# Kernel optimization log

Measured on AMD Instinct MI355X. Metric: run time of the kernel, lower is better.

Reference implementation:

```python
import jax, jax.numpy as jnp
import numpy as np

N_NODES = 30522
HID = 768
N_EDGES = 488352
B, S = 4, 512
L = 12  # transformer_layers
C = 100  # num classes in pos-neg codebook graph


def setup_inputs() -> dict:
    key = jax.random.key(0)
    ks = jax.random.split(key, 20)
    inp = {}
    inp["word_embs"] = jax.random.normal(ks[0], (N_NODES, HID), dtype=jnp.float32)
    inp["input_ids"] = jax.random.randint(ks[1], (B, S), 0, N_NODES + 1)  # N_NODES = padding row
    inp["class_ids"] = jax.random.randint(ks[2], (B, S), 0, C + 1)
    inp["mask"] = jax.random.randint(ks[3], (B, S, 1), 0, 2).astype(bool)
    inp["co_edge_index"] = jax.random.randint(ks[4], (2, N_EDGES), 0, N_NODES)
    inp["co_edge_weight"] = jax.random.uniform(ks[5], (N_EDGES,), dtype=jnp.float32)
    inp["re_edge_index"] = jax.random.randint(ks[6], (2, N_EDGES), 0, N_NODES)
    inp["re_edge_weight"] = jax.random.uniform(ks[7], (N_EDGES,), dtype=jnp.float32)
    pn_graph = jax.random.uniform(ks[8], (C + 1, N_NODES), dtype=jnp.float32) * 0.01
    inp["pn_graph"] = pn_graph.at[-1].set(0.0)  # padding row of zeros
    sc = 0.02
    inp["co_W"] = jax.random.normal(ks[9], (3, HID, HID), dtype=jnp.float32) * sc
    inp["co_b"] = jnp.zeros((3, HID), jnp.float32)
    inp["re_W"] = jax.random.normal(ks[10], (3, HID, HID), dtype=jnp.float32) * sc
    inp["re_b"] = jnp.zeros((3, HID), jnp.float32)
    inp["pn_W"] = jax.random.normal(ks[11], (HID, HID), dtype=jnp.float32) * sc  # [out,in] 1x1 conv
    inp["pn_b"] = jnp.zeros((HID,), jnp.float32)
    # zero_convs are zero-initialized in the original; use small random so math is non-trivial
    inp["zero_w"] = jax.random.normal(ks[12], (L, HID, HID), dtype=jnp.float32) * sc
    inp["zero_b"] = jnp.zeros((L, HID), jnp.float32)
    inp["zero_w_pos"] = jax.random.normal(ks[13], (L, HID, HID), dtype=jnp.float32) * sc
    inp["zero_b_pos"] = jnp.zeros((L, HID), jnp.float32)
    return inp


def _gcn_layer(x, src, dst, ew, W, b, n):
    # PyG GCNConv: add self-loops (weight 1), symmetric normalization
    deg = jax.ops.segment_sum(ew, dst, num_segments=n) + 1.0
    dinv = jnp.where(deg > 0, jax.lax.rsqrt(deg), 0.0)
    norm = dinv[src] * ew * dinv[dst]  # [E]
    h = x @ W  # [n, H]
    agg = jax.ops.segment_sum(norm[:, None] * h[src], dst, num_segments=n)
    agg = agg + h * (dinv * dinv)[:, None]  # self-loop contribution
    return agg + b


def _gcn_stack(x, edge_index, ew, Ws, bs, ids):
    src, dst = edge_index[0], edge_index[1]
    n = x.shape[0]
    h = x
    acc = None
    for i in range(3):
        h = jax.nn.relu(_gcn_layer(h, src, dst, ew, Ws[i], bs[i], n))
        pad = jnp.concatenate([h, jnp.zeros((1, h.shape[-1]), h.dtype)], axis=0)
        g = pad[ids]  # [B, S, H] gather with padding row
        acc = g if acc is None else acc + g
    return acc / 3.0


def _zero_conv_layers(tok, w, b):
    # 1x1 conv over hidden channels for each of L layers: [B,S,H] x [L,O,H] -> [L,B,S,O]
    return jnp.einsum("bsh,loh->lbso", tok, w) + b[:, None, None, :]


def reference(word_embs, input_ids, class_ids, mask,
              co_edge_index, co_edge_weight, re_edge_index, re_edge_weight,
              pn_graph, co_W, co_b, re_W, re_b, pn_W, pn_b,
              zero_w, zero_b, zero_w_pos, zero_b_pos):
    Bq, Sq = input_ids.shape
    H = word_embs.shape[-1]
    Lq = zero_w.shape[0]
    inv_mask = (~mask).astype(word_embs.dtype)  # [B,S,1]
    zero_pad = jnp.zeros((Lq, Bq, 1, H), word_embs.dtype)

    co = _gcn_stack(word_embs, co_edge_index, co_edge_weight, co_W, co_b, input_ids)  # [B,S,H]
    re = _gcn_stack(word_embs, re_edge_index, re_edge_weight, re_W, re_b, input_ids)

    # NOTE: original uses self.zero_convs (not a separate set) for BOTH co and re
    co_l = _zero_conv_layers(co, zero_w, zero_b) * inv_mask[None]
    re_l = _zero_conv_layers(re, zero_w, zero_b) * inv_mask[None]
    co_l = jnp.concatenate([zero_pad, co_l], axis=2)  # [L,B,S+1,H]
    re_l = jnp.concatenate([zero_pad, re_l], axis=2)

    # PosNegCodebook: 1x1 conv on codebook, then dense-graph matmul, gathered by class
    cb = word_embs @ pn_W.T + pn_b  # [N, H]
    pn = (pn_graph @ cb)[class_ids]  # [B,S,H] (same math as graph[class_ids] @ cb)
    pn_l = _zero_conv_layers(pn, zero_w_pos, zero_b_pos)
    pn_l = jnp.concatenate([zero_pad, pn_l], axis=2)

    return (co_l, re_l, pn_l)
```

## Files before the change

kernel.cpp:

```cpp
#include <hip/hip_runtime.h>
#include <stdint.h>

typedef unsigned int u32;
typedef unsigned short u16;
typedef __attribute__((ext_vector_type(8))) short short8;
typedef __attribute__((ext_vector_type(4))) float f32x4;

#define N_NODESC 30522
#define HIDC 768
#define NEC 488352
#define TOKM 2048
#define LLAY 12
#define NCLS 101
#define M_PAD 30720
#define ZNC (LLAY*HIDC)
#define OUT_SET (LLAY*4*513*HIDC)
#define PN_KCHUNK 512
#define NBLK 120
#define NN1 (N_NODESC+1)
#define G4_LDS 65536
#define G8_LDS 131072

__device__ __forceinline__ float bl(u32 u){ return __uint_as_float(u<<16); }
__device__ __forceinline__ float bh(u32 u){ return __uint_as_float(u & 0xffff0000u); }
__device__ __forceinline__ u32 f2b1(float f){ u32 x=__float_as_uint(f); return (x + 0x7fffu + ((x>>16)&1u))>>16; }
__device__ __forceinline__ u32 pack2(float a, float b){ return f2b1(a) | (f2b1(b)<<16); }

__device__ __forceinline__ void mfma16(f32x4& d, short8 a, short8 b){
  asm volatile("v_mfma_f32_16x16x32_bf16 %0, %1, %2, %0" : "+v"(d) : "v"(a), "v"(b));
}
__device__ __forceinline__ void async16(const void* g, void* l){
  __builtin_amdgcn_global_load_lds((const __attribute__((address_space(1))) u32*)g,
                                   (__attribute__((address_space(3))) u32*)l, 16, 0, 0);
}

__global__ void k_invmask(const void* __restrict__ mask, float* __restrict__ invm){
  __shared__ int s_byte, s_flt;
  int t = threadIdx.x;
  const unsigned char* mb = (const unsigned char*)mask;
  const u32* mw = (const u32*)mask;
  int lb=0, lf=0;
  for(int i=t;i<2048;i+=256) if((i&3)!=0 && mb[i]!=0) lb=1;
  for(int i=t;i<512;i+=256) if(mw[i]==0x3F800000u) lf=1;
  if(t==0){ s_byte=0; s_flt=0; }
  __syncthreads();
  if(lb) s_byte=1;
  if(lf) s_flt=1;
  __syncthreads();
  int mode = s_flt ? 2 : (s_byte ? 1 : 0);
  for(int p=t;p<2048;p+=256){
    int mv = (mode==1) ? (int)mb[p] : (int)(mw[p]!=0u);
    invm[p] = mv ? 0.f : 1.f;
  }
}

__global__ void k_needed(const int* __restrict__ ids, u32* __restrict__ needed){
  int p = blockIdx.x*256 + threadIdx.x;
  if(p < TOKM){ int id = ids[p]; if(id < N_NODESC) needed[id] = 1u; }
}

__global__ void k_need1_init(const u32* __restrict__ needed, u32* __restrict__ need1){
  int v = blockIdx.x*256 + threadIdx.x;
  if(v < N_NODESC){ u32 x = needed[v]; need1[v] = x; need1[N_NODESC + v] = x; }
}
__global__ void k_need_expand(const int* __restrict__ coei, const int* __restrict__ reei,
                              const u32* __restrict__ needed, u32* __restrict__ need1){
  int g = blockIdx.y;
  const int* ei = g ? reei : coei;
  int e = blockIdx.x*256 + threadIdx.x;
  if(e < NEC){
    int d = ei[NEC+e];
    if(needed[d]) need1[(size_t)g*N_NODESC + ei[e]] = 1u;
  }
}

__global__ void k_conv(const float* __restrict__ src, u16* __restrict__ dst, int ndw){
  int i = blockIdx.x*256 + threadIdx.x;
  if(i < ndw) ((u32*)dst)[i] = pack2(src[2*i], src[2*i+1]);
}
__global__ void k_conv_pad(const float* __restrict__ src, u16* __restrict__ dst, int srcRows, int padRows){
  int i = blockIdx.x*256 + threadIdx.x;
  if(i >= padRows*384) return;
  int row = i/384; int c2 = (i - row*384)*2;
  float lo=0.f, hi=0.f;
  if(row < srcRows){ const float* s = src + (size_t)row*HIDC + c2; lo=s[0]; hi=s[1]; }
  ((u32*)dst)[i] = pack2(lo, hi);
}
__global__ void k_pnb(const float* __restrict__ png, u16* __restrict__ pnb){
  int i = blockIdx.x*256 + threadIdx.x;
  if(i >= 128*(M_PAD/2)) return;
  int row = i/(M_PAD/2); int k2 = (i - row*(M_PAD/2))*2;
  float lo=0.f, hi=0.f;
  if(row < NCLS){
    const float* s = png + (size_t)row*N_NODESC;
    if(k2 < N_NODESC) lo = s[k2];
    if(k2+1 < N_NODESC) hi = s[k2+1];
  }
  ((u32*)pnb)[i] = pack2(lo, hi);
}
__global__ void k_transposeW2(const float* __restrict__ coW, const float* __restrict__ reW,
                              u16* __restrict__ Wt2){
  int g = blockIdx.y;
  int i = blockIdx.x*256 + threadIdx.x;
  if(i >= 3*HIDC*384) return;
  const float* W = g ? reW : coW;
  int mat = i/(HIDC*384); int rem = i - mat*HIDC*384;
  int n = rem/384; int kd = rem - n*384;
  const float* Wm = W + (size_t)mat*HIDC*HIDC;
  float lo = Wm[(size_t)(2*kd)*HIDC + n];
  float hi = Wm[(size_t)(2*kd+1)*HIDC + n];
  ((u32*)Wt2)[(size_t)g*3*HIDC*384 + (size_t)mat*HIDC*384 + (size_t)n*384 + kd] = pack2(lo, hi);
}

__global__ void k_degcnt2(const int* __restrict__ coei, const int* __restrict__ reei,
                          const float* __restrict__ coew, const float* __restrict__ reew,
                          float* __restrict__ deg2, int* __restrict__ cnt2){
  int g = blockIdx.y;
  const int* ei = g ? reei : coei;
  const float* ew = g ? reew : coew;
  int e = blockIdx.x*256 + threadIdx.x;
  if(e < NEC){ int d = ei[NEC+e]; atomicAdd(&deg2[(size_t)g*N_NODESC + d], ew[e]); atomicAdd(&cnt2[(size_t)g*N_NODESC + d], 1); }
}
__global__ void k_dinv2(const float* __restrict__ deg2, float* __restrict__ dinvA, float* __restrict__ dinvB){
  int g = blockIdx.y;
  int v = blockIdx.x*256 + threadIdx.x;
  if(v < N_NODESC){
    float d = deg2[(size_t)g*N_NODESC + v] + 1.f;
    dinvA[(size_t)g*N_NODESC + v] = rsqrtf(d);
    dinvB[(size_t)g*N_NODESC + v] = 1.f/d;
  }
}
__global__ void k_scan1(const int* __restrict__ cnt2, int* __restrict__ part2){
  __shared__ int wt[4];
  int g = blockIdx.y, b = blockIdx.x, t = threadIdx.x;
  int lane = t & 63, w = t >> 6;
  int i = b*256 + t;
  int v = (i < N_NODESC) ? cnt2[(size_t)g*N_NODESC + i] : 0;
  int x = v;
  #pragma unroll
  for(int off=1; off<64; off<<=1){ int y = __shfl_up(x, off); if(lane>=off) x += y; }
  if(lane==63) wt[w] = x;
  __syncthreads();
  if(t==0) part2[g*NBLK + b] = wt[0]+wt[1]+wt[2]+wt[3];
}
__global__ void k_scan2(int* __restrict__ part2, int* __restrict__ rp2){
  __shared__ int w0tot;
  int g = blockIdx.x, t = threadIdx.x;
  int lane = t & 63, w = t >> 6;
  int v = (t < NBLK) ? part2[g*NBLK + t] : 0;
  int x = v;
  #pragma unroll
  for(int off=1; off<64; off<<=1){ int y = __shfl_up(x, off); if(lane>=off) x += y; }
  if(w==0 && lane==63) w0tot = x;
  __syncthreads();
  int incl = x + (w ? w0tot : 0);
  int excl = incl - v;
  if(t < NBLK) part2[g*NBLK + t] = excl;
  if(t == 127) rp2[(size_t)g*NN1 + N_NODESC] = incl;
}
__global__ void k_scan3(const int* __restrict__ cnt2, const int* __restrict__ part2,
                        int* __restrict__ rp2, int* __restrict__ cur2){
  __shared__ int wt[4];
  int g = blockIdx.y, b = blockIdx.x, t = threadIdx.x;
  int lane = t & 63, w = t >> 6;
  int i = b*256 + t;
  int v = (i < N_NODESC) ? cnt2[(size_t)g*N_NODESC + i] : 0;
  int x = v;
  #pragma unroll
  for(int off=1; off<64; off<<=1){ int y = __shfl_up(x, off); if(lane>=off) x += y; }
  if(lane==63) wt[w] = x;
  __syncthreads();
  int wpre = 0;
  #pragma unroll
  for(int j=0;j<4;j++) if(j<w) wpre += wt[j];
  int excl = x - v + wpre + part2[g*NBLK + b];
  if(i < N_NODESC){ rp2[(size_t)g*NN1 + i] = excl; cur2[(size_t)g*N_NODESC + i] = excl; }
}
__global__ void k_scatter2(const int* __restrict__ coei, const int* __restrict__ reei,
                           const float* __restrict__ coew, const float* __restrict__ reew,
                           const float* __restrict__ dinvA, int* __restrict__ cur2,
                           float2* __restrict__ emeta){
  int g = blockIdx.y;
  const int* ei = g ? reei : coei;
  const float* ew = g ? reew : coew;
  int e = blockIdx.x*256 + threadIdx.x;
  if(e < NEC){
    int s = ei[e], d = ei[NEC+e];
    int pos = atomicAdd(&cur2[(size_t)g*N_NODESC + d], 1);
    float nrm = dinvA[(size_t)g*N_NODESC + s]*ew[e]*dinvA[(size_t)g*N_NODESC + d];
    emeta[(size_t)g*NEC + pos] = make_float2(__int_as_float(s), nrm);
  }
}

__global__ __launch_bounds__(256)
void k_spmm(const u16* __restrict__ hW, const int* __restrict__ rp,
            const float2* __restrict__ emeta, const float* __restrict__ dinv2,
            const float* __restrict__ bias, u16* __restrict__ hout,
            const u32* __restrict__ needed){
  int v = blockIdx.x*4 + (threadIdx.x>>6);
  if(v >= N_NODESC) return;
  if(needed && !needed[v]) return;
  int lane = threadIdx.x & 63;
  const u32* H = (const u32*)hW;
  float acc[12];
  #pragma unroll
  for(int q=0;q<12;q++) acc[q]=0.f;
  int e0 = rp[v], e1 = rp[v+1];
  int e = e0;
  for(; e+4<=e1; e+=4){
    float2 m0=emeta[e], m1=emeta[e+1], m2=emeta[e+2], m3=emeta[e+3];
    const u32* r0 = H + (size_t)__float_as_int(m0.x)*384 + lane;
    const u32* r1 = H + (size_t)__float_as_int(m1.x)*384 + lane;
    const u32* r2 = H + (size_t)__float_as_int(m2.x)*384 + lane;
    const u32* r3 = H + (size_t)__float_as_int(m3.x)*384 + lane;
    u32 u0[6],u1[6],u2[6],u3[6];
    #pragma unroll
    for(int q=0;q<6;q++){ u0[q]=r0[q*64]; u1[q]=r1[q*64]; u2[q]=r2[q*64]; u3[q]=r3[q*64]; }
    #pragma unroll
    for(int q=0;q<6;q++){
      acc[2*q]   += m0.y*bl(u0[q]) + m1.y*bl(u1[q]) + m2.y*bl(u2[q]) + m3.y*bl(u3[q]);
      acc[2*q+1] += m0.y*bh(u0[q]) + m1.y*bh(u1[q]) + m2.y*bh(u2[q]) + m3.y*bh(u3[q]);
    }
  }
  for(; e<e1; ++e){
    float2 mm = emeta[e];
    const u32* r = H + (size_t)__float_as_int(mm.x)*384 + lane;
    #pragma unroll
    for(int q=0;q<6;q++){ u32 u = r[q*64]; acc[2*q] += mm.y*bl(u); acc[2*q+1] += mm.y*bh(u); }
  }
  { float wgt = dinv2[v];
    const u32* r = H + (size_t)v*384 + lane;
    #pragma unroll
    for(int q=0;q<6;q++){ u32 u = r[q*64]; acc[2*q] += wgt*bl(u); acc[2*q+1] += wgt*bh(u); }
  }
  const float2* B2 = (const float2*)bias;
  u32* O = (u32*)hout + (size_t)v*384 + lane;
  #pragma unroll
  for(int q=0;q<6;q++){
    float2 bb = B2[lane + 64*q];
    float x0 = fmaxf(acc[2*q]+bb.x, 0.f);
    float x1 = fmaxf(acc[2*q+1]+bb.y, 0.f);
    O[q*64] = pack2(x0, x1);
  }
}

__global__ void k_gather(const u16* __restrict__ h, const int* __restrict__ ids,
                         float2* __restrict__ tokf, u16* __restrict__ tokb, int phase){
  int d = blockIdx.x*256 + threadIdx.x;
  if(d >= TOKM*384) return;
  int p = d/384, q = d - p*384;
  int id = ids[p];
  float x0=0.f, x1=0.f;
  if(id < N_NODESC){ u32 u = ((const u32*)h)[(size_t)id*384 + q]; x0 = bl(u)*(1.f/3.f); x1 = bh(u)*(1.f/3.f); }
  float2 cur;
  if(phase==0){ cur.x=x0; cur.y=x1; }
  else { cur = tokf[d]; cur.x += x0; cur.y += x1; }
  if(phase==2) ((u32*)tokb)[d] = pack2(cur.x, cur.y);
  else tokf[d] = cur;
}

__global__ void k_gather_pn(const float* __restrict__ GT, const int* __restrict__ cids, u16* __restrict__ tokb){
  int d = blockIdx.x*256 + threadIdx.x;
  if(d >= TOKM*384) return;
  int p = d/384, q = d - p*384;
  int cid = cids[p];
  float lo = GT[(size_t)(2*q)*128 + cid];
  float hi = GT[(size_t)(2*q+1)*128 + cid];
  ((u32*)tokb)[d] = pack2(lo, hi);
}

__global__ void k_zerocol(float* __restrict__ out){
  int i = blockIdx.x*256 + threadIdx.x;
  if(i >= 3*LLAY*4*HIDC) return;
  int set = i/(LLAY*4*HIDC); int rem = i - set*(LLAY*4*HIDC);
  int l = rem/(4*HIDC); int rem2 = rem - l*(4*HIDC);
  int b = rem2/HIDC; int o = rem2 - b*HIDC;
  out[(size_t)set*OUT_SET + (size_t)(l*4+b)*513*HIDC + o] = 0.f;
}

__device__ __forceinline__ void g_split(int ntM, int ntN, int& bm, int& bn){
  int nwg = ntM*ntN;
  int bid = (int)blockIdx.x;
  int wg = (bid & 7)*(nwg>>3) + (bid>>3);
  if(ntN <= ntM){ bm = wg/ntN; bn = wg - bm*ntN; }
  else          { bn = wg/ntM; bm = wg - bn*ntM; }
}

#define G8_AOFF(b) ((b)*65536)
#define G8_BOFF(b) ((b)*65536 + 32768)

__device__ __forceinline__ void g8_stage(const u16* __restrict__ src, int ldk, int g0, int kt,
                                         char* half_base, int tid){
  const int lane = tid & 63;
  const int csw = ((lane&7) ^ (lane>>3)) << 3;
  const u16* s0 = src + (size_t)(g0 + (tid>>3))*ldk + (kt + csw);
  const u16* s1 = src + (size_t)(g0 + 64 + (tid>>3))*ldk + (kt + csw);
  async16(s0, half_base + (size_t)tid*16);
  async16(s1, half_base + 8192 + (size_t)tid*16);
}

__device__ __forceinline__ void g8_core(const u16* __restrict__ A, const u16* __restrict__ Bt,
                                        int K, int m0, int n0,
                                        f32x4 (&acc)[8][4], char* LDS, int tid){
  const int lane = tid & 63;
  const int wid = tid >> 6;
  const int wr = wid >> 2, wc = wid & 3;
  const int NK = K >> 6;

  g8_stage(Bt, K, n0,      0, LDS + G8_BOFF(0),         tid);
  g8_stage(Bt, K, n0+128,  0, LDS + G8_BOFF(0) + 16384, tid);
  g8_stage(A,  K, m0,      0, LDS + G8_AOFF(0),         tid);
  g8_stage(A,  K, m0+128,  0, LDS + G8_AOFF(0) + 16384, tid);
  g8_stage(Bt, K, n0,     64, LDS + G8_BOFF(1),         tid);
  g8_stage(Bt, K, n0+128, 64, LDS + G8_BOFF(1) + 16384, tid);
  asm volatile("s_waitcnt vmcnt(4)" ::: "memory");
  __builtin_amdgcn_sched_barrier(0);
  __builtin_amdgcn_s_barrier();
  __builtin_amdgcn_sched_barrier(0);

  short8 bf8[8];
  for(int T=0; T<NK; ++T){
    const int buf = T & 1;
    const char* Ab = LDS + G8_AOFF(buf) + wr*16384;
    const char* Bb = LDS + G8_BOFF(buf) + (wc>>1)*16384;
    #pragma unroll
    for(int q=0; q<4; ++q){
      if(q==0){
        #pragma unroll
        for(int n=0;n<4;n++){
          #pragma unroll
          for(int kk=0;kk<2;kk++){
            int row = ((wc&1)<<6) + (n<<4) + (lane&15);
            int cb = ((kk<<6) + ((lane>>4)<<4)) ^ ((lane&7)<<4);
            bf8[n*2+kk] = *(const short8*)(Bb + row*128 + cb);
          }
        }
      }
      short8 af[2][2];
      #pragma unroll
      for(int j=0;j<2;j++){
        #pragma unroll
        for(int kk=0;kk<2;kk++){
          int row = ((2*q+j)<<4) + (lane&15);
          int cb = ((kk<<6) + ((lane>>4)<<4)) ^ ((lane&7)<<4);
          af[j][kk] = *(const short8*)(Ab + row*128 + cb);
        }
      }
      if(q==0 && T+1<NK) g8_stage(A,  K, m0,      (T+1)<<6, LDS + G8_AOFF((T+1)&1),         tid);
      if(q==1 && T+1<NK) g8_stage(A,  K, m0+128,  (T+1)<<6, LDS + G8_AOFF((T+1)&1) + 16384, tid);
      if(q==2 && T+2<NK) g8_stage(Bt, K, n0,      (T+2)<<6, LDS + G8_BOFF(buf),             tid);
      if(q==3 && T+2<NK) g8_stage(Bt, K, n0+128,  (T+2)<<6, LDS + G8_BOFF(buf) + 16384,     tid);
      if(q==3){
        if(T <= NK-3)      asm volatile("s_waitcnt vmcnt(4)" ::: "memory");
        else if(T == NK-2) asm volatile("s_waitcnt vmcnt(0)" ::: "memory");
      }
      __builtin_amdgcn_sched_barrier(0);
      __builtin_amdgcn_s_barrier();
      __builtin_amdgcn_sched_barrier(0);
      __builtin_amdgcn_s_setprio(1);
      #pragma unroll
      for(int j=0;j<2;j++){
        #pragma unroll
        for(int n=0;n<4;n++){
          #pragma unroll
          for(int kk=0;kk<2;kk++) mfma16(acc[2*q+j][n], af[j][kk], bf8[n*2+kk]);
        }
      }
      __builtin_amdgcn_s_setprio(0);
      __builtin_amdgcn_sched_barrier(0);
      __builtin_amdgcn_s_barrier();
      __builtin_amdgcn_sched_barrier(0);
    }
  }
}

__global__ __launch_bounds__(512,2)
void gemm8p_zc(const u16* __restrict__ TOKALL, const u16* __restrict__ ZWALL,
               const float* __restrict__ zb, const float* __restrict__ zbp,
               const float* __restrict__ invm, float* __restrict__ out){
  extern __shared__ char LDS[];
  const int set = blockIdx.z;
  const u16* A  = TOKALL + (size_t)set*TOKM*HIDC;
  const u16* Bt = ZWALL + (set==2 ? (size_t)ZNC*HIDC : 0);
  const float* bias = (set==2) ? zbp : zb;
  const bool use_mask = (set != 2);
  float* o = out + (size_t)set*OUT_SET;

  const int tid = threadIdx.x;
  const int lane = tid & 63;
  const int wid = tid >> 6;
  const int wr = wid >> 2, wc = wid & 3;
  int bm, bn;
  g_split(TOKM>>8, ZNC>>8, bm, bn);
  const int m0 = bm << 8, n0 = bn << 8;

  f32x4 acc[8][4];
  f32x4 zv = {0.f,0.f,0.f,0.f};
  #pragma unroll
  for(int m=0;m<8;m++){
    #pragma unroll
    for(int n=0;n<4;n++) acc[m][n] = zv;
  }
  g8_core(A, Bt, HIDC, m0, n0, acc, LDS, tid);

  const int l = n0 / HIDC;
  const int oc0 = n0 - l*HIDC;
  const int lo = lane & 15, hi = lane >> 4;

  #pragma unroll
  for(int pass=0; pass<2; ++pass){
    __syncthreads();
    if(wr == pass){
      #pragma unroll
      for(int m=0;m<8;m++){
        #pragma unroll
        for(int n=0;n<4;n++){
          int col = (wc<<6) + (n<<4) + lo;
          float badd = bias[n0 + col];
          #pragma unroll
          for(int r=0;r<4;r++){
            int lr = (m<<4) + (hi<<2) + r;
            *(float*)(LDS + (size_t)lr*1024 + ((col<<2) ^ ((lr&7)<<4))) = acc[m][n][r] + badd;
          }
        }
      }
    }
    __syncthreads();
    #pragma unroll
    for(int i=0;i<16;i++){
      int lr = (i<<3) + wid;
      int rr = m0 + (pass<<7) + lr;
      int b = rr >> 9, s = rr & 511;
      f32x4 v = *(const f32x4*)(LDS + (size_t)lr*1024 + ((lane<<4) ^ ((lr&7)<<4)));
      if(use_mask){ float w = invm[rr]; v = v * w; }
      *(f32x4*)(o + (size_t)((l*4+b)*513 + (s+1))*HIDC + oc0 + (lane<<2)) = v;
    }
  }
}

#define G4_ABUF(b) ((b)*32768)
#define G4_BBUF(b) ((b)*32768 + 16384)

__device__ __forceinline__ void g4_stage(const u16* __restrict__ src, int ldk, int g0, int kt,
                                         char* base, int tid){
  const int lane = tid & 63;
  const int csw = ((lane&7) ^ (lane>>3)) << 3;
  const int r = tid >> 3;
  #pragma unroll
  for(int h=0; h<4; ++h)
    async16(src + (size_t)(g0 + h*32 + r)*ldk + (kt + csw), base + h*4096 + (size_t)tid*16);
}

__device__ __forceinline__ void g4_core(const u16* __restrict__ A, const u16* __restrict__ Bt,
                                        int K, int m0, int n0,
                                        f32x4 (&acc)[4][4], char* LDS, int tid){
  const int lane = tid & 63;
  const int wid = tid >> 6;
  const int wr = wid >> 1, wc = wid & 1;
  const int NK = K >> 6;

  g4_stage(A,  K, m0,  0, LDS + G4_ABUF(0), tid);
  g4_stage(Bt, K, n0,  0, LDS + G4_BBUF(0), tid);
  g4_stage(A,  K, m0, 64, LDS + G4_ABUF(1), tid);
  g4_stage(Bt, K, n0, 64, LDS + G4_BBUF(1), tid);

  short8 af[4][2], bf[4][2];
  for(int T=0; T<NK; ++T){
    const int buf = T & 1;
    const char* Ab = LDS + G4_ABUF(buf) + wr*8192;
    const char* Bb = LDS + G4_BBUF(buf) + wc*8192;
    if(T+1 < NK) asm volatile("s_waitcnt vmcnt(8)" ::: "memory");
    else         asm volatile("s_waitcnt vmcnt(0)" ::: "memory");
    __builtin_amdgcn_sched_barrier(0);
    __builtin_amdgcn_s_barrier();
    __builtin_amdgcn_sched_barrier(0);
    #pragma unroll
    for(int m=0;m<4;m++){
      #pragma unroll
      for(int kk=0;kk<2;kk++){
        int row = (m<<4) + (lane&15);
        int cb = ((kk<<6) + ((lane>>4)<<4)) ^ ((lane&7)<<4);
        af[m][kk] = *(const short8*)(Ab + row*128 + cb);
        bf[m][kk] = *(const short8*)(Bb + row*128 + cb);
      }
    }
    asm volatile("s_waitcnt lgkmcnt(0)" ::: "memory");
    __builtin_amdgcn_sched_barrier(0);
    __builtin_amdgcn_s_setprio(1);
    #pragma unroll
    for(int m=0;m<2;m++){
      #pragma unroll
      for(int n=0;n<4;n++){
        #pragma unroll
        for(int kk=0;kk<2;kk++) mfma16(acc[m][n], af[m][kk], bf[n][kk]);
      }
    }
    __builtin_amdgcn_s_setprio(0);
    __builtin_amdgcn_sched_barrier(0);
    __builtin_amdgcn_s_barrier();
    __builtin_amdgcn_sched_barrier(0);
    if(T+2 < NK){
      g4_stage(A,  K, m0, (T+2)<<6, LDS + G4_ABUF(buf), tid);
      g4_stage(Bt, K, n0, (T+2)<<6, LDS + G4_BBUF(buf), tid);
    }
    __builtin_amdgcn_s_setprio(1);
    #pragma unroll
    for(int m=2;m<4;m++){
      #pragma unroll
      for(int n=0;n<4;n++){
        #pragma unroll
        for(int kk=0;kk<2;kk++) mfma16(acc[m][n], af[m][kk], bf[n][kk]);
      }
    }
    __builtin_amdgcn_s_setprio(0);
    __builtin_amdgcn_sched_barrier(0);
  }
}

template<int MODE>
__global__ __launch_bounds__(256,2)
void gemm4p_bf16(const u16* __restrict__ A, const u16* __restrict__ Bt,
                 int M, int N, int K,
                 u16* __restrict__ outB, const float* __restrict__ bias){
  extern __shared__ char LDS[];
  const int tid = threadIdx.x;
  const int lane = tid & 63;
  const int wid = tid >> 6;
  const int wr = wid >> 1, wc = wid & 1;
  int bm, bn;
  g_split(M>>7, N>>7, bm, bn);
  const int m0 = bm << 7, n0 = bn << 7;

  f32x4 acc[4][4];
  f32x4 zv = {0.f,0.f,0.f,0.f};
  #pragma unroll
  for(int m=0;m<4;m++){
    #pragma unroll
    for(int n=0;n<4;n++) acc[m][n] = zv;
  }
  g4_core(A, Bt, K, m0, n0, acc, LDS, tid);

  const int rbase = (lane>>4)<<2;
  const int cbase = lane & 15;
  #pragma unroll
  for(int m=0;m<4;m++){
    int row0 = m0 + (wr<<6) + (m<<4) + rbase;
    #pragma unroll
    for(int n=0;n<4;n++){
      int col = n0 + (wc<<6) + (n<<4) + cbase;
      #pragma unroll
      for(int r=0;r<4;r++){
        float v = acc[m][n][r];
        if(MODE==2) v += bias[row0+r];
        outB[(size_t)(row0+r)*N + col] = (u16)f2b1(v);
      }
    }
  }
}

__global__ __launch_bounds__(256,2)
void gemm_splitk(const u16* __restrict__ A, const u16* __restrict__ Bt,
                 int M, int N, int K, float* __restrict__ outF, int kchunk){
  __shared__ u16 As[128*64];
  __shared__ u16 Bs[128*64];
  const int t = threadIdx.x;
  const int lane = t & 63;
  const int w = t >> 6;
  const int wr = w >> 1, wc = w & 1;
  int nchunks = (K + kchunk - 1)/kchunk;
  int bm = (int)blockIdx.x / nchunks;
  int ch = (int)blockIdx.x - bm*nchunks;
  int k0 = ch*kchunk, k1 = k0 + kchunk; if(k1 > K) k1 = K;
  const int m0 = bm << 7, n0 = 0;

  f32x4 zv = {0.f,0.f,0.f,0.f};
  f32x4 acc[4][4];
  #pragma unroll
  for(int m=0;m<4;m++){
    #pragma unroll
    for(int n=0;n<4;n++) acc[m][n] = zv;
  }
  const int srow = t >> 3;
  const int scol = (t & 7) << 3;
  const u16* Ag = A + (size_t)(m0 + srow)*K + scol;
  const u16* Bg = Bt + (size_t)(n0 + srow)*K + scol;
  u16* Al = &As[t*8];
  u16* Bl = &Bs[t*8];

  for(int kt=k0; kt<k1; kt+=64){
    __syncthreads();
    #pragma unroll
    for(int i=0;i<4;i++){
      async16(Ag + (size_t)(i*32)*K + kt, Al + i*2048);
      async16(Bg + (size_t)(i*32)*K + kt, Bl + i*2048);
    }
    __syncthreads();
    #pragma unroll
    for(int kk=0; kk<64; kk+=32){
      const int ko = kk + ((lane>>4)<<3);
      short8 af[4], bfv[4];
      #pragma unroll
      for(int m=0;m<4;m++) af[m] = *(const short8*)&As[((wr<<6)+(m<<4)+(lane&15))*64 + ko];
      #pragma unroll
      for(int n=0;n<4;n++) bfv[n] = *(const short8*)&Bs[((wc<<6)+(n<<4)+(lane&15))*64 + ko];
      #pragma unroll
      for(int m=0;m<4;m++){
        #pragma unroll
        for(int n=0;n<4;n++) mfma16(acc[m][n], af[m], bfv[n]);
      }
    }
  }
  const int rbase = (lane>>4)<<2;
  const int cbase = lane & 15;
  #pragma unroll
  for(int m=0;m<4;m++){
    int row0 = m0 + (wr<<6) + (m<<4) + rbase;
    #pragma unroll
    for(int n=0;n<4;n++){
      int col = n0 + (wc<<6) + (n<<4) + cbase;
      #pragma unroll
      for(int r=0;r<4;r++) atomicAdd(&outF[(size_t)(row0+r)*N + col], acc[m][n][r]);
    }
  }
}

extern "C" void kernel_launch(void* const* d_in, const int* in_sizes, int n_in,
                              void* d_out, int out_size, void* d_ws, size_t ws_size,
                              hipStream_t stream){
  const float* word  = (const float*)d_in[0];
  const int*   ids   = (const int*)d_in[1];
  const int*   cids  = (const int*)d_in[2];
  const void*  mask  = d_in[3];
  const int*   co_ei = (const int*)d_in[4];
  const float* co_ew = (const float*)d_in[5];
  const int*   re_ei = (const int*)d_in[6];
  const float* re_ew = (const float*)d_in[7];
  const float* png   = (const float*)d_in[8];
  const float* co_W  = (const float*)d_in[9];
  const float* co_b  = (const float*)d_in[10];
  const float* re_W  = (const float*)d_in[11];
  const float* re_b  = (const float*)d_in[12];
  const float* pn_W  = (const float*)d_in[13];
  const float* pn_b  = (const float*)d_in[14];
  const float* zw    = (const float*)d_in[15];
  const float* zb    = (const float*)d_in[16];
  const float* zwp   = (const float*)d_in[17];
  const float* zbp   = (const float*)d_in[18];
  float* out = (float*)d_out;

  hipFuncSetAttribute((const void*)gemm4p_bf16<0>, hipFuncAttributeMaxDynamicSharedMemorySize, G4_LDS);
  hipFuncSetAttribute((const void*)gemm4p_bf16<2>, hipFuncAttributeMaxDynamicSharedMemorySize, G4_LDS);
  hipFuncSetAttribute((const void*)gemm8p_zc,      hipFuncAttributeMaxDynamicSharedMemorySize, G8_LDS);

  char* wsb = (char*)d_ws;
  size_t off = 0;
  auto alloc = [&](size_t bytes)->void*{ void* p = wsb + off; off += (bytes + 255) & ~(size_t)255; return p; };
  u16* WORDB = (u16*)alloc((size_t)M_PAD*HIDC*2);
  u16* BUFB  = (u16*)alloc((size_t)M_PAD*HIDC*2);
  u16* BUFX  = (u16*)alloc((size_t)M_PAD*HIDC*2);
  u16* ZWALL = (u16*)alloc((size_t)2*ZNC*HIDC*2);
  u16* WT2   = (u16*)alloc((size_t)2*3*HIDC*HIDC*2);
  u16* PNWB  = (u16*)alloc((size_t)HIDC*HIDC*2);
  u16* PNB   = (u16*)alloc((size_t)128*M_PAD*2);
  u16* TOKALL= (u16*)alloc((size_t)3*TOKM*HIDC*2);
  float2* TOKF = (float2*)alloc((size_t)TOKM*HIDC*4);
  float* GT   = (float*)alloc((size_t)HIDC*128*4);
  float* DEG2 = (float*)alloc((size_t)2*N_NODESC*4);
  int*   CNT2 = (int*)alloc((size_t)2*N_NODESC*4);
  float* DINVA = (float*)alloc((size_t)2*N_NODESC*4);
  float* DINVB = (float*)alloc((size_t)2*N_NODESC*4);
  int*   RP2  = (int*)alloc((size_t)2*NN1*4);
  int*   CUR2 = (int*)alloc((size_t)2*N_NODESC*4);
  int*   PART2= (int*)alloc((size_t)2*NBLK*4);
  float2* EMETA=(float2*)alloc((size_t)2*NEC*8);
  u32*   NEED = (u32*)alloc((size_t)N_NODESC*4);
  u32*   NEED1= (u32*)alloc((size_t)2*N_NODESC*4);
  float* INVM = (float*)alloc((size_t)TOKM*4);
  (void)ws_size; (void)in_sizes; (void)n_in; (void)out_size;

  const int GD_TOK = (TOKM*384 + 255)/256;
  const int GD_E   = (NEC + 255)/256;
  const int GD_N   = (N_NODESC + 255)/256;
  const int SPMM_GD  = (N_NODESC + 3)/4;
  const int PN_NCHUNKS = M_PAD/PN_KCHUNK;
  const int G_PN  = (HIDC/128)*PN_NCHUNKS;
  const int G4_GCN = (M_PAD/128)*(HIDC/128);
  const int G4_CBT = (HIDC/128)*(M_PAD/128);
  const int G8_ZC  = (TOKM/256)*(ZNC/256);

  hipMemsetAsync(NEED, 0, (size_t)N_NODESC*4, stream);
  hipMemsetAsync(DEG2, 0, (size_t)2*N_NODESC*4, stream);
  hipMemsetAsync(CNT2, 0, (size_t)2*N_NODESC*4, stream);
  k_invmask<<<1,256,0,stream>>>(mask, INVM);
  k_needed<<<(TOKM+255)/256,256,0,stream>>>(ids, NEED);
  k_need1_init<<<GD_N,256,0,stream>>>(NEED, NEED1);
  k_need_expand<<<dim3(GD_E,2),256,0,stream>>>(co_ei, re_ei, NEED, NEED1);
  k_conv<<<(HIDC*HIDC/2 + 255)/256,256,0,stream>>>(pn_W, PNWB, HIDC*HIDC/2);
  k_conv<<<(ZNC*HIDC/2 + 255)/256,256,0,stream>>>(zw, ZWALL, ZNC*HIDC/2);
  k_conv<<<(ZNC*HIDC/2 + 255)/256,256,0,stream>>>(zwp, ZWALL + (size_t)ZNC*HIDC, ZNC*HIDC/2);
  k_conv_pad<<<(M_PAD*384 + 255)/256,256,0,stream>>>(word, WORDB, N_NODESC, M_PAD);
  k_transposeW2<<<dim3((3*HIDC*384 + 255)/256, 2),256,0,stream>>>(co_W, re_W, WT2);

  k_degcnt2<<<dim3(GD_E,2),256,0,stream>>>(co_ei, re_ei, co_ew, re_ew, DEG2, CNT2);
  k_dinv2<<<dim3(GD_N,2),256,0,stream>>>(DEG2, DINVA, DINVB);
  k_scan1<<<dim3(NBLK,2),256,0,stream>>>(CNT2, PART2);
  k_scan2<<<2,128,0,stream>>>(PART2, RP2);
  k_scan3<<<dim3(NBLK,2),256,0,stream>>>(CNT2, PART2, RP2, CUR2);
  k_scatter2<<<dim3(GD_E,2),256,0,stream>>>(co_ei, re_ei, co_ew, re_ew, DINVA, CUR2, EMETA);

  gemm4p_bf16<2><<<G4_CBT,256,G4_LDS,stream>>>(PNWB, WORDB, HIDC, M_PAD, HIDC, BUFX, pn_b);
  k_pnb<<<(128*(M_PAD/2) + 255)/256,256,0,stream>>>(png, PNB);
  hipMemsetAsync(GT, 0, (size_t)HIDC*128*4, stream);
  gemm_splitk<<<G_PN,256,0,stream>>>(BUFX, PNB, HIDC, 128, M_PAD, GT, PN_KCHUNK);
  k_gather_pn<<<GD_TOK,256,0,stream>>>(GT, cids, TOKALL + (size_t)2*TOKM*HIDC);

  auto run_graph = [&](int g, const float* bf, u16* tokb){
    const int* rp = RP2 + (size_t)g*NN1;
    const float2* em = EMETA + (size_t)g*NEC;
    const float* di2 = DINVB + (size_t)g*N_NODESC;
    const u16* X = WORDB;
    for(int i=0;i<3;i++){
      gemm4p_bf16<0><<<G4_GCN,256,G4_LDS,stream>>>(X, WT2 + ((size_t)g*3 + i)*HIDC*HIDC,
                                                   M_PAD, HIDC, HIDC, BUFB, nullptr);
      const u32* flt = (i==2) ? NEED : (i==1 ? NEED1 + (size_t)g*N_NODESC : nullptr);
      k_spmm<<<SPMM_GD,256,0,stream>>>(BUFB, rp, em, di2, bf + i*HIDC, BUFX, flt);
      k_gather<<<GD_TOK,256,0,stream>>>(BUFX, ids, TOKF, tokb, i);
      X = BUFX;
    }
  };
  run_graph(0, co_b, TOKALL);
  run_graph(1, re_b, TOKALL + (size_t)TOKM*HIDC);

  dim3 zgrid(G8_ZC, 1, 3);
  gemm8p_zc<<<zgrid,512,G8_LDS,stream>>>(TOKALL, ZWALL, zb, zbp, INVM, out);
  k_zerocol<<<(3*LLAY*4*HIDC + 255)/256,256,0,stream>>>(out);
}
```

Before: 1.140 ms.

## Fuse token gather into SpMM via node-to-token linked lists

Builds a per-node linked list of token positions (atomicExch into a node map plus a next array), so each SpMM wavefront writes its result straight into the token accumulation buffers. This removes the separate gather kernels. On the last layer it also skips writing the full node output. The two zero-conv weight conversions are merged into one launch, and the token bf16 buffers are zeroed up front so padding tokens stay zero. The cost is an atomic-built list, serial per-node chain walks, and extra token read-modify-write work inside the SpMM.

```diff
diff --git a/kernel.cpp b/kernel.cpp
--- a/kernel.cpp
+++ b/kernel.cpp
@@ -54,9 +54,17 @@
   }
 }
 
-__global__ void k_needed(const int* __restrict__ ids, u32* __restrict__ needed){
+__global__ void k_needed(const int* __restrict__ ids, u32* __restrict__ needed,
+                         int* __restrict__ tmap, int* __restrict__ nxt){
   int p = blockIdx.x*256 + threadIdx.x;
-  if(p < TOKM){ int id = ids[p]; if(id < N_NODESC) needed[id] = 1u; }
+  if(p < TOKM){
+    int id = ids[p];
+    if(id < N_NODESC){
+      needed[id] = 1u;
+      int old = atomicExch(&tmap[id], p);
+      nxt[p] = old;
+    }
+  }
 }
 
 __global__ void k_need1_init(const u32* __restrict__ needed, u32* __restrict__ need1){
@@ -77,6 +85,14 @@
 __global__ void k_conv(const float* __restrict__ src, u16* __restrict__ dst, int ndw){
   int i = blockIdx.x*256 + threadIdx.x;
   if(i < ndw) ((u32*)dst)[i] = pack2(src[2*i], src[2*i+1]);
+}
+__global__ void k_conv2(const float* __restrict__ a, const float* __restrict__ b,
+                        u16* __restrict__ dst, int ndwHalf){
+  int i = blockIdx.x*256 + threadIdx.x;
+  if(i >= 2*ndwHalf) return;
+  const float* s = (i < ndwHalf) ? a : b;
+  int j = (i < ndwHalf) ? i : i - ndwHalf;
+  ((u32*)dst)[i] = pack2(s[2*j], s[2*j+1]);
 }
 __global__ void k_conv_pad(const float* __restrict__ src, u16* __restrict__ dst, int srcRows, int padRows){
   int i = blockIdx.x*256 + threadIdx.x;
@@ -196,7 +212,9 @@
 void k_spmm(const u16* __restrict__ hW, const int* __restrict__ rp,
             const float2* __restrict__ emeta, const float* __restrict__ dinv2,
             const float* __restrict__ bias, u16* __restrict__ hout,
-            const u32* __restrict__ needed){
+            const u32* __restrict__ needed,
+            const int* __restrict__ tmap, const int* __restrict__ nxt,
+            float2* __restrict__ tokf, u16* __restrict__ tokb, int phase){
   int v = blockIdx.x*4 + (threadIdx.x>>6);
   if(v >= N_NODESC) return;
   if(needed && !needed[v]) return;
@@ -234,29 +252,44 @@
     for(int q=0;q<6;q++){ u32 u = r[q*64]; acc[2*q] += wgt*bl(u); acc[2*q+1] += wgt*bh(u); }
   }
   const float2* B2 = (const float2*)bias;
-  u32* O = (u32*)hout + (size_t)v*384 + lane;
+  u32 wv[6];
   #pragma unroll
   for(int q=0;q<6;q++){
     float2 bb = B2[lane + 64*q];
     float x0 = fmaxf(acc[2*q]+bb.x, 0.f);
     float x1 = fmaxf(acc[2*q+1]+bb.y, 0.f);
-    O[q*64] = pack2(x0, x1);
-  }
-}
-
-__global__ void k_gather(const u16* __restrict__ h, const int* __restrict__ ids,
-                         float2* __restrict__ tokf, u16* __restrict__ tokb, int phase){
-  int d = blockIdx.x*256 + threadIdx.x;
-  if(d >= TOKM*384) return;
-  int p = d/384, q = d - p*384;
-  int id = ids[p];
-  float x0=0.f, x1=0.f;
-  if(id < N_NODESC){ u32 u = ((const u32*)h)[(size_t)id*384 + q]; x0 = bl(u)*(1.f/3.f); x1 = bh(u)*(1.f/3.f); }
-  float2 cur;
-  if(phase==0){ cur.x=x0; cur.y=x1; }
-  else { cur = tokf[d]; cur.x += x0; cur.y += x1; }
-  if(phase==2) ((u32*)tokb)[d] = pack2(cur.x, cur.y);
-  else tokf[d] = cur;
+    wv[q] = pack2(x0, x1);
+  }
+  if(phase != 2){
+    u32* O = (u32*)hout + (size_t)v*384 + lane;
+    #pragma unroll
+    for(int q=0;q<6;q++) O[q*64] = wv[q];
+  }
+  int p = tmap[v];
+  while(p >= 0){
+    float2* TF = tokf + (size_t)p*384 + lane;
+    if(phase == 0){
+      #pragma unroll
+      for(int q=0;q<6;q++)
+        TF[q*64] = make_float2(bl(wv[q])*(1.f/3.f), bh(wv[q])*(1.f/3.f));
+    } else if(phase == 1){
+      #pragma unroll
+      for(int q=0;q<6;q++){
+        float2 c = TF[q*64];
+        c.x += bl(wv[q])*(1.f/3.f); c.y += bh(wv[q])*(1.f/3.f);
+        TF[q*64] = c;
+      }
+    } else {
+      u32* TB = (u32*)tokb + (size_t)p*384 + lane;
+      #pragma unroll
+      for(int q=0;q<6;q++){
+        float2 c = TF[q*64];
+        c.x += bl(wv[q])*(1.f/3.f); c.y += bh(wv[q])*(1.f/3.f);
+        TB[q*64] = pack2(c.x, c.y);
+      }
+    }
+    p = nxt[p];
+  }
 }
 
 __global__ void k_gather_pn(const float* __restrict__ GT, const int* __restrict__ cids, u16* __restrict__ tokb){
@@ -675,6 +708,8 @@
   float2* EMETA=(float2*)alloc((size_t)2*NEC*8);
   u32*   NEED = (u32*)alloc((size_t)N_NODESC*4);
   u32*   NEED1= (u32*)alloc((size_t)2*N_NODESC*4);
+  int*   TMAP = (int*)alloc((size_t)N_NODESC*4);
+  int*   NXT  = (int*)alloc((size_t)TOKM*4);
   float* INVM = (float*)alloc((size_t)TOKM*4);
   (void)ws_size; (void)in_sizes; (void)n_in; (void)out_size;
 
@@ -689,15 +724,16 @@
   const int G8_ZC  = (TOKM/256)*(ZNC/256);
 
   hipMemsetAsync(NEED, 0, (size_t)N_NODESC*4, stream);
+  hipMemsetAsync(TMAP, 0xFF, (size_t)N_NODESC*4, stream);
   hipMemsetAsync(DEG2, 0, (size_t)2*N_NODESC*4, stream);
   hipMemsetAsync(CNT2, 0, (size_t)2*N_NODESC*4, stream);
+  hipMemsetAsync(TOKALL, 0, (size_t)2*TOKM*HIDC*2, stream);
   k_invmask<<<1,256,0,stream>>>(mask, INVM);
-  k_needed<<<(TOKM+255)/256,256,0,stream>>>(ids, NEED);
+  k_needed<<<(TOKM+255)/256,256,0,stream>>>(ids, NEED, TMAP, NXT);
   k_need1_init<<<GD_N,256,0,stream>>>(NEED, NEED1);
   k_need_expand<<<dim3(GD_E,2),256,0,stream>>>(co_ei, re_ei, NEED, NEED1);
   k_conv<<<(HIDC*HIDC/2 + 255)/256,256,0,stream>>>(pn_W, PNWB, HIDC*HIDC/2);
-  k_conv<<<(ZNC*HIDC/2 + 255)/256,256,0,stream>>>(zw, ZWALL, ZNC*HIDC/2);
-  k_conv<<<(ZNC*HIDC/2 + 255)/256,256,0,stream>>>(zwp, ZWALL + (size_t)ZNC*HIDC, ZNC*HIDC/2);
+  k_conv2<<<(2*(ZNC*HIDC/2) + 255)/256,256,0,stream>>>(zw, zwp, ZWALL, ZNC*HIDC/2);
   k_conv_pad<<<(M_PAD*384 + 255)/256,256,0,stream>>>(word, WORDB, N_NODESC, M_PAD);
   k_transposeW2<<<dim3((3*HIDC*384 + 255)/256, 2),256,0,stream>>>(co_W, re_W, WT2);
 
@@ -723,8 +759,8 @@
       gemm4p_bf16<0><<<G4_GCN,256,G4_LDS,stream>>>(X, WT2 + ((size_t)g*3 + i)*HIDC*HIDC,
                                                    M_PAD, HIDC, HIDC, BUFB, nullptr);
       const u32* flt = (i==2) ? NEED : (i==1 ? NEED1 + (size_t)g*N_NODESC : nullptr);
-      k_spmm<<<SPMM_GD,256,0,stream>>>(BUFB, rp, em, di2, bf + i*HIDC, BUFX, flt);
-      k_gather<<<GD_TOK,256,0,stream>>>(BUFX, ids, TOKF, tokb, i);
+      k_spmm<<<SPMM_GD,256,0,stream>>>(BUFB, rp, em, di2, bf + i*HIDC, BUFX, flt,
+                                       TMAP, NXT, TOKF, tokb, i);
       X = BUFX;
     }
   };
```

Result: no change. 1.129 ms (-0.9%).
